# Optimization experiments

Measured on AMD Instinct MI355X. Metric: run time of the kernel, lower is better.

The kernel has to match this reference:

```python
import jax, jax.numpy as jnp
import numpy as np

EPS = 1e-5

# ---------------- numpy-side hash/index precomputation ----------------

def _key(c):
    c = c.astype(np.int64) + 2  # shift so all coords >= 0
    return (c[..., 0] * 4096 + c[..., 1]) * 4096 + c[..., 2]

def _lookup(table_keys, query_keys):
    order = np.argsort(table_keys)
    sk = table_keys[order]
    pos = np.clip(np.searchsorted(sk, query_keys), 0, len(sk) - 1)
    found = sk[pos] == query_keys
    return np.where(found, order[pos], -1).astype(np.int64)

def setup_inputs() -> dict:
    N, C_IN, C_OUT, RES = 400_000, 32, 64, 1.0
    rng = np.random.default_rng(0)
    coords = rng.uniform(0.0, 100.0, (N, 3)).astype(np.float32)
    pf = rng.standard_normal((N, C_IN)).astype(np.float32)

    # initial_voxelize: unique voxel coords + point->voxel map
    vc = np.floor(coords / RES).astype(np.int64)
    uv, p2v_in = np.unique(vc, axis=0, return_inverse=True)
    p2v_in = p2v_in.reshape(-1)
    cnt_in = np.bincount(p2v_in, minlength=len(uv)).astype(np.float32)

    # strided conv output lattice (stride 2)
    ouv = np.unique(uv // 2, axis=0)
    ikeys, okeys = _key(uv), _key(ouv)

    # kernel-2 stride-2 conv map: input voxel at 2*out + off, off in {0,1}^3
    offs2 = np.array([[i, j, k] for i in (0, 1) for j in (0, 1) for k in (0, 1)], np.int64)
    conv_map = np.stack([_lookup(ikeys, _key(ouv * 2 + o)) for o in offs2], axis=1)

    # kernel-3 neighbor map on the output lattice
    offs3 = np.array([[i, j, k] for i in (-1, 0, 1) for j in (-1, 0, 1) for k in (-1, 0, 1)], np.int64)
    nbr27 = np.stack([_lookup(okeys, _key(ouv + o)) for o in offs3], axis=1)

    # trilinear voxel_to_point on output lattice (voxel size = 2*RES)
    q = coords / (2.0 * RES)
    base = np.floor(q).astype(np.int64)
    frac = (q - base).astype(np.float32)
    tri_idx, tri_w = [], []
    for o in offs2:
        idx = _lookup(okeys, _key(base + o))
        w = np.prod(np.where(o[None, :] == 1, frac, 1.0 - frac), axis=1).astype(np.float32)
        tri_idx.append(idx)
        tri_w.append(np.where(idx >= 0, w, 0.0).astype(np.float32))
    tri_idx = np.stack(tri_idx, axis=1)
    tri_w = np.stack(tri_w, axis=1)

    # point_to_voxel: containing output voxel (always exists)
    p2v_out = _lookup(okeys, _key(base))
    cnt_out = np.bincount(p2v_out, minlength=len(ouv)).astype(np.float32)

    def glorot(r, *shape):
        fan_in = shape[-2] * int(np.prod(shape[:-2])) if len(shape) > 2 else shape[0]
        return (r.standard_normal(shape) / np.sqrt(fan_in)).astype(np.float32)

    return dict(
        pf=jnp.asarray(pf),
        Wc=jnp.asarray(glorot(rng, 8, C_IN, C_OUT)),
        g1=jnp.ones(C_OUT, jnp.float32), b1=jnp.zeros(C_OUT, jnp.float32),
        Wr1=jnp.asarray(glorot(rng, 27, C_OUT, C_OUT)),
        gr1=jnp.ones(C_OUT, jnp.float32), br1=jnp.zeros(C_OUT, jnp.float32),
        Wr2=jnp.asarray(glorot(rng, 27, C_OUT, C_OUT)),
        gr2=jnp.ones(C_OUT, jnp.float32), br2=jnp.zeros(C_OUT, jnp.float32),
        Wpt=jnp.asarray(glorot(rng, C_OUT, C_OUT)), bpt=jnp.zeros(C_OUT, jnp.float32),
        gp=jnp.ones(C_OUT, jnp.float32), bp=jnp.zeros(C_OUT, jnp.float32),
        tri_w=jnp.asarray(tri_w), cnt_in=jnp.asarray(cnt_in), cnt_out=jnp.asarray(cnt_out),
        p2v_in=jnp.asarray(p2v_in), conv_map=jnp.asarray(conv_map),
        nbr27=jnp.asarray(nbr27), tri_idx=jnp.asarray(tri_idx), p2v_out=jnp.asarray(p2v_out),
    )

# ---------------- jax forward ----------------

def _bn(x, g, b):  # training-mode batch norm over voxel/point dim
    m = x.mean(0)
    v = x.var(0)
    return (x - m) * jax.lax.rsqrt(v + EPS) * g + b

def _seg_mean(x, seg, cnt):  # spvoxelize: scatter-mean
    return jax.ops.segment_sum(x, seg, num_segments=cnt.shape[0]) / cnt[:, None]

def _sconv(f, nbr, W):  # sparse conv: per-offset gather + matmul accumulate
    out = jnp.zeros((nbr.shape[0], W.shape[2]), f.dtype)
    for k in range(W.shape[0]):
        idx = nbr[:, k]
        g = jnp.where((idx >= 0)[:, None], f[jnp.maximum(idx, 0)], 0.0)
        out = out + g @ W[k]
    return out

def _tri(f, idx, w):  # trilinear voxel->point gather (w already 0 for missing)
    out = jnp.zeros((idx.shape[0], f.shape[1]), f.dtype)
    for j in range(idx.shape[1]):
        out = out + w[:, j:j + 1] * f[jnp.maximum(idx[:, j], 0)]
    return out

def reference(pf, Wc, g1, b1, Wr1, gr1, br1, Wr2, gr2, br2, Wpt, bpt, gp, bp,
              tri_w, cnt_in, cnt_out, p2v_in, conv_map, nbr27, tri_idx, p2v_out):
    vf0 = _seg_mean(pf, p2v_in, cnt_in)                         # initial_voxelize [M_in,32]
    vf1 = jax.nn.relu(_bn(_sconv(vf0, conv_map, Wc), g1, b1))   # conv_in [M_out,64]
    pfeat = _tri(vf1, tri_idx, tri_w)                           # voxel_to_point [N,64]
    vf2 = _seg_mean(pfeat, p2v_out, cnt_out)                    # point_to_voxel [M_out,64]
    h = jax.nn.relu(_bn(_sconv(vf2, nbr27, Wr1), gr1, br1))     # ResBlock conv1
    h = jax.nn.relu(_bn(_sconv(h, nbr27, Wr2), gr2, br2))       # ResBlock conv2
    vf3 = h + vf2                                               # residual sum
    p_out = jax.nn.relu(_bn(pfeat @ Wpt + bpt, gp, bp))         # point_layer
    pfeat2 = _tri(vf3, tri_idx, tri_w) + p_out                  # v2p + fuse
    vf4 = _seg_mean(pfeat2, p2v_out, cnt_out)                   # point_to_voxel
    return vf4, pfeat2
```

## Files before the change

### kernel.cpp

```cpp
#include <hip/hip_runtime.h>

#define EPSV 1e-5f
#define CDIV(a, b) (((a) + (b) - 1) / (b))

using short8 = __attribute__((ext_vector_type(8))) short;
using f32x4 = __attribute__((ext_vector_type(4))) float;

__device__ __forceinline__ unsigned short bf16rne(float x) {
  unsigned u = __float_as_uint(x);
  unsigned r = (u + 0x7fffu + ((u >> 16) & 1u)) >> 16;
  return (unsigned short)r;
}

__global__ __launch_bounds__(256) void k_conv1(const float* __restrict__ vin,
                                               const int* __restrict__ cmap,
                                               const float* __restrict__ W,
                                               float* __restrict__ out,
                                               float* __restrict__ stats, int Vout) {
  __shared__ float fs[32][128];
  __shared__ float Ws[32 * 64];
  __shared__ int idxs[128 * 8];
  __shared__ float ss[128];
  const int tid = threadIdx.x;
  const int vb = blockIdx.x * 128;
  for (int i = tid; i < 128 * 8; i += 256) {
    int g = vb * 8 + i;
    idxs[i] = (g < Vout * 8) ? cmap[g] : -1;
  }
  if (tid < 128) ss[tid] = 0.f;
  const int vq = tid & 15, cq = tid >> 4;
  const int v0 = vq * 8, c0 = cq * 4;
  const int srow = tid & 127, sci = (tid >> 7) * 16;
  float acc[8][4];
#pragma unroll
  for (int r = 0; r < 8; ++r)
#pragma unroll
    for (int q = 0; q < 4; ++q) acc[r][q] = 0.f;

  for (int k = 0; k < 8; ++k) {
    __syncthreads();
    for (int i = tid; i < 32 * 64; i += 256) Ws[i] = W[k * 2048 + i];
    int idx = idxs[srow * 8 + k];
    if (idx >= 0) {
#pragma unroll
      for (int j = 0; j < 16; j += 4) {
        float4 t = *(const float4*)&vin[(size_t)idx * 32 + sci + j];
        fs[sci + j + 0][srow] = t.x;
        fs[sci + j + 1][srow] = t.y;
        fs[sci + j + 2][srow] = t.z;
        fs[sci + j + 3][srow] = t.w;
      }
    } else {
#pragma unroll
      for (int j = 0; j < 16; ++j) fs[sci + j][srow] = 0.f;
    }
    __syncthreads();
#pragma unroll 8
    for (int ci = 0; ci < 32; ++ci) {
      float4 w4 = *(const float4*)&Ws[ci * 64 + c0];
      float4 fa = *(const float4*)&fs[ci][v0];
      float4 fb = *(const float4*)&fs[ci][v0 + 4];
      float fv[8] = {fa.x, fa.y, fa.z, fa.w, fb.x, fb.y, fb.z, fb.w};
      float wv[4] = {w4.x, w4.y, w4.z, w4.w};
#pragma unroll
      for (int r = 0; r < 8; ++r)
#pragma unroll
        for (int q = 0; q < 4; ++q) acc[r][q] += fv[r] * wv[q];
    }
  }
  float s1[4] = {0, 0, 0, 0}, s2[4] = {0, 0, 0, 0};
#pragma unroll
  for (int r = 0; r < 8; ++r) {
    int v = vb + v0 + r;
    if (v < Vout) {
      *(float4*)&out[(size_t)v * 64 + c0] =
          make_float4(acc[r][0], acc[r][1], acc[r][2], acc[r][3]);
#pragma unroll
      for (int q = 0; q < 4; ++q) {
        float x = acc[r][q];
        s1[q] += x;
        s2[q] += x * x;
      }
    }
  }
#pragma unroll
  for (int q = 0; q < 4; ++q) {
    atomicAdd(&ss[c0 + q], s1[q]);
    atomicAdd(&ss[64 + c0 + q], s2[q]);
  }
  __syncthreads();
  if (tid < 128) atomicAdd(&stats[tid], ss[tid]);
}

__global__ void k_bnfin(const float* __restrict__ stats, const float* __restrict__ g,
                        const float* __restrict__ b, float* __restrict__ sb, int rows) {
  int c = threadIdx.x;
  float inv = 1.f / (float)rows;
  float m = stats[c] * inv;
  float v = stats[64 + c] * inv - m * m;
  float sc = g[c] * rsqrtf(v + EPSV);
  sb[c] = sc;
  sb[64 + c] = b[c] - m * sc;
}

__global__ __launch_bounds__(1024) void k_scan_part(const float* __restrict__ cnt,
                                                    int* __restrict__ partial, int V) {
  __shared__ int s[1024];
  int i = blockIdx.x * 1024 + threadIdx.x;
  s[threadIdx.x] = (i < V) ? (int)cnt[i] : 0;
  __syncthreads();
  for (int st = 512; st > 0; st >>= 1) {
    if (threadIdx.x < st) s[threadIdx.x] += s[threadIdx.x + st];
    __syncthreads();
  }
  if (threadIdx.x == 0) partial[blockIdx.x] = s[0];
}

__global__ __launch_bounds__(1024) void k_scan_top(int* __restrict__ partial, int nb) {
  __shared__ int s[1024];
  int t = threadIdx.x;
  int orig = (t < nb) ? partial[t] : 0;
  s[t] = orig;
  __syncthreads();
  for (int st = 1; st < 1024; st <<= 1) {
    int v = (t >= st) ? s[t - st] : 0;
    __syncthreads();
    s[t] += v;
    __syncthreads();
  }
  if (t < nb) partial[t] = s[t] - orig;
}

__global__ __launch_bounds__(1024) void k_scan_write(const float* __restrict__ cnt,
                                                     const int* __restrict__ partial,
                                                     int* __restrict__ starts,
                                                     int* __restrict__ cursor, int V) {
  __shared__ int s[1024];
  int t = threadIdx.x;
  int i = blockIdx.x * 1024 + t;
  int orig = (i < V) ? (int)cnt[i] : 0;
  s[t] = orig;
  __syncthreads();
  for (int st = 1; st < 1024; st <<= 1) {
    int v = (t >= st) ? s[t - st] : 0;
    __syncthreads();
    s[t] += v;
    __syncthreads();
  }
  if (i < V) {
    int excl = s[t] - orig + partial[blockIdx.x];
    starts[i] = excl;
    cursor[i] = excl;
  }
}

__global__ void k_bucket(const int* __restrict__ p2v, int* __restrict__ cursor,
                         int* __restrict__ plist, int N) {
  int p = blockIdx.x * 256 + threadIdx.x;
  if (p >= N) return;
  int pos = atomicAdd(&cursor[p2v[p]], 1);
  plist[pos] = p;
}

__global__ __launch_bounds__(256) void k_seg_gather_in(const float* __restrict__ src,
                                                       const int* __restrict__ starts,
                                                       const float* __restrict__ cnt,
                                                       const int* __restrict__ plist,
                                                       float* __restrict__ dst, int V) {
  int t = threadIdx.x;
  int v = blockIdx.x * 8 + (t >> 5);
  int c = t & 31;
  if (v >= V) return;
  int s0 = starts[v];
  int n = (int)cnt[v];
  float acc = 0.f;
  for (int i = 0; i < n; ++i) acc += src[(size_t)plist[s0 + i] * 32 + c];
  dst[(size_t)v * 32 + c] = acc / (float)n;
}

__global__ __launch_bounds__(256) void k_tri1v(const float* __restrict__ c1,
                                               const float* __restrict__ sb0,
                                               const int* __restrict__ tidx,
                                               const float* __restrict__ twt,
                                               const int* __restrict__ starts,
                                               const float* __restrict__ cnt,
                                               const int* __restrict__ plist,
                                               float* __restrict__ pfeat,
                                               float* __restrict__ vf2, int V) {
  int t = threadIdx.x;
  int v = blockIdx.x * 4 + (t >> 6);
  int c = t & 63;
  if (v >= V) return;
  int s0 = starts[v];
  int n = (int)cnt[v];
  if (n < 1) return;
  int p0 = plist[s0];
  float sc = sb0[c], bi = sb0[64 + c];
  float R[8];
#pragma unroll
  for (int j = 0; j < 8; ++j) {
    int idx = tidx[(size_t)p0 * 8 + j];
    R[j] = (idx >= 0) ? fmaxf(sc * c1[(size_t)idx * 64 + c] + bi, 0.f) : 0.f;
  }
  float acc_v = 0.f;
  for (int i = 0; i < n; ++i) {
    int p = plist[s0 + i];
    float4 w0 = *(const float4*)&twt[(size_t)p * 8];
    float4 w1 = *(const float4*)&twt[(size_t)p * 8 + 4];
    float acc = w0.x * R[0] + w0.y * R[1] + w0.z * R[2] + w0.w * R[3] +
                w1.x * R[4] + w1.y * R[5] + w1.z * R[6] + w1.w * R[7];
    pfeat[(size_t)p * 64 + c] = acc;
    acc_v += acc;
  }
  vf2[(size_t)v * 64 + c] = acc_v / (float)n;
}

__global__ void k_wprep(const float* __restrict__ W, short* __restrict__ Wh,
                        short* __restrict__ Wl, int ntap) {
  int t = blockIdx.x * 256 + threadIdx.x;
  int total = ntap * 2 * 4 * 64;
  if (t >= total) return;
  int l = t & 63;
  int n = (t >> 6) & 3;
  int s = (t >> 8) & 1;
  int k = t >> 9;
  int co = n * 16 + (l & 15);
  int ci0 = s * 32 + (l >> 4) * 8;
#pragma unroll
  for (int j = 0; j < 8; ++j) {
    float x = W[((size_t)(k * 64 + ci0 + j)) * 64 + co];
    unsigned short hb = bf16rne(x);
    float hf = __uint_as_float((unsigned)hb << 16);
    Wh[(size_t)t * 8 + j] = (short)hb;
    Wl[(size_t)t * 8 + j] = (short)bf16rne(x - hf);
  }
}

__global__ void k_split(const float* __restrict__ in, const float* __restrict__ sb,
                        short* __restrict__ packed, int total) {
  int i = blockIdx.x * 256 + threadIdx.x;
  if (i >= total) return;
  int c = i & 63;
  float x = in[i];
  if (sb) x = fmaxf(sb[c] * x + sb[64 + c], 0.f);
  unsigned short hb = bf16rne(x);
  float hf = __uint_as_float((unsigned)hb << 16);
  size_t base = (size_t)(i >> 6) * 128 + c;
  packed[base] = (short)hb;
  packed[base + 64] = (short)bf16rne(x - hf);
}

__global__ __launch_bounds__(128) void k_conv27r(const short* __restrict__ A_g,
                                                 const int* __restrict__ nbr,
                                                 const short* __restrict__ Wh,
                                                 const short* __restrict__ Wl,
                                                 float* __restrict__ out,
                                                 float* __restrict__ stats, int Vout,
                                                 int nwg) {
  __shared__ float ss[128];
  const int tid = threadIdx.x;
  const int lane = tid & 63;
  const int w = tid >> 6;
  int bid = blockIdx.x;
  int q = nwg >> 3, r = nwg & 7;
  int xcd = bid & 7, pos = bid >> 3;
  int swz = (xcd < r ? xcd * (q + 1) : r * (q + 1) + (xcd - r) * q) + pos;
  const int vb = swz * 64 + w * 32;
  ss[tid] = 0.f;
  const int vv = lane & 15, kq = lane >> 4;
  const int v0 = vb + vv, v1 = vb + 16 + vv;
  const bool ok0 = v0 < Vout, ok1 = v1 < Vout;
  const int koff = kq * 8;

  f32x4 acc[2][4];
#pragma unroll
  for (int m = 0; m < 2; ++m)
#pragma unroll
    for (int n = 0; n < 4; ++n)
#pragma unroll
      for (int rr = 0; rr < 4; ++rr) acc[m][n][rr] = 0.f;

  auto ldA = [&](int idx, int off) -> short8 {
    if (idx < 0) {
      short8 z = 0;
      return z;
    }
    return *(const short8*)&A_g[(size_t)idx * 128 + off];
  };

  short8 cA[8], nA[8];
  int idn0, idn1;

  {
    int i0 = ok0 ? nbr[(size_t)v0 * 27] : -1;
    int i1 = ok1 ? nbr[(size_t)v1 * 27] : -1;
#pragma unroll
    for (int s = 0; s < 2; ++s)
#pragma unroll
      for (int h = 0; h < 2; ++h) {
        cA[s * 2 + h] = ldA(i0, h * 64 + s * 32 + koff);
        cA[4 + s * 2 + h] = ldA(i1, h * 64 + s * 32 + koff);
      }
    idn0 = ok0 ? nbr[(size_t)v0 * 27 + 1] : -1;
    idn1 = ok1 ? nbr[(size_t)v1 * 27 + 1] : -1;
  }

  for (int k = 0; k < 27; ++k) {
    int idf0 = -1, idf1 = -1;
    if (k + 1 < 27) {
#pragma unroll
      for (int s = 0; s < 2; ++s)
#pragma unroll
        for (int h = 0; h < 2; ++h) {
          nA[s * 2 + h] = ldA(idn0, h * 64 + s * 32 + koff);
          nA[4 + s * 2 + h] = ldA(idn1, h * 64 + s * 32 + koff);
        }
      if (k + 2 < 27) {
        idf0 = ok0 ? nbr[(size_t)v0 * 27 + (k + 2)] : -1;
        idf1 = ok1 ? nbr[(size_t)v1 * 27 + (k + 2)] : -1;
      }
    }
    const short* bkh = Wh + (size_t)k * 4096 + lane * 8;
    const short* bkl = Wl + (size_t)k * 4096 + lane * 8;
#pragma unroll
    for (int s = 0; s < 2; ++s) {
      short8 ah0 = cA[s * 2], al0 = cA[s * 2 + 1];
      short8 ah1 = cA[4 + s * 2], al1 = cA[4 + s * 2 + 1];
#pragma unroll
      for (int n = 0; n < 4; ++n) {
        short8 bh = *(const short8*)&bkh[(s * 4 + n) * 512];
        short8 bl = *(const short8*)&bkl[(s * 4 + n) * 512];
        acc[0][n] = __builtin_amdgcn_mfma_f32_16x16x32_bf16(ah0, bh, acc[0][n], 0, 0, 0);
        acc[0][n] = __builtin_amdgcn_mfma_f32_16x16x32_bf16(al0, bh, acc[0][n], 0, 0, 0);
        acc[0][n] = __builtin_amdgcn_mfma_f32_16x16x32_bf16(ah0, bl, acc[0][n], 0, 0, 0);
        acc[1][n] = __builtin_amdgcn_mfma_f32_16x16x32_bf16(ah1, bh, acc[1][n], 0, 0, 0);
        acc[1][n] = __builtin_amdgcn_mfma_f32_16x16x32_bf16(al1, bh, acc[1][n], 0, 0, 0);
        acc[1][n] = __builtin_amdgcn_mfma_f32_16x16x32_bf16(ah1, bl, acc[1][n], 0, 0, 0);
      }
    }
    if (k + 1 < 27) {
#pragma unroll
      for (int qq = 0; qq < 8; ++qq) cA[qq] = nA[qq];
      idn0 = idf0;
      idn1 = idf1;
    }
  }

  const int col = lane & 15, rq = lane >> 4;
  __syncthreads();
#pragma unroll
  for (int m = 0; m < 2; ++m) {
#pragma unroll
    for (int n = 0; n < 4; ++n) {
      int c = n * 16 + col;
      float s1 = 0.f, s2 = 0.f;
#pragma unroll
      for (int rr = 0; rr < 4; ++rr) {
        int v = vb + w * 0 + m * 16 + rq * 4 + rr;
        if (v < Vout) {
          float x = acc[m][n][rr];
          out[(size_t)v * 64 + c] = x;
          s1 += x;
          s2 += x * x;
        }
      }
      atomicAdd(&ss[c], s1);
      atomicAdd(&ss[64 + c], s2);
    }
  }
  __syncthreads();
  atomicAdd(&stats[tid], ss[tid]);
}

__global__ void k_vf3(const float* __restrict__ h2, const float* __restrict__ vf2,
                      const float* __restrict__ sb2, float* __restrict__ vf3, int total) {
  int i = blockIdx.x * 256 + threadIdx.x;
  if (i >= total) return;
  int c = i & 63;
  vf3[i] = fmaxf(sb2[c] * h2[i] + sb2[64 + c], 0.f) + vf2[i];
}

__global__ __launch_bounds__(256) void k_pmm(const float* __restrict__ pfeat,
                                             const float* __restrict__ Wpt,
                                             const float* __restrict__ bpt,
                                             float* __restrict__ outbuf,
                                             float* __restrict__ stats, int N) {
  __shared__ float fs[64][128];
  __shared__ float Ws[64 * 64];
  __shared__ float ss[128];
  const int tid = threadIdx.x;
  const int pb = blockIdx.x * 128;
  for (int i = tid; i < 64 * 64; i += 256) Ws[i] = Wpt[i];
  if (tid < 128) ss[tid] = 0.f;
  const int srow = tid & 127, sci = (tid >> 7) * 32;
  int p = pb + srow;
  if (p < N) {
#pragma unroll
    for (int j = 0; j < 32; j += 4) {
      float4 t = *(const float4*)&pfeat[(size_t)p * 64 + sci + j];
      fs[sci + j + 0][srow] = t.x;
      fs[sci + j + 1][srow] = t.y;
      fs[sci + j + 2][srow] = t.z;
      fs[sci + j + 3][srow] = t.w;
    }
  } else {
#pragma unroll
    for (int j = 0; j < 32; ++j) fs[sci + j][srow] = 0.f;
  }
  __syncthreads();
  const int vq = tid & 15, cq = tid >> 4;
  const int p0 = vq * 8, c0 = cq * 4;
  float acc[8][4];
#pragma unroll
  for (int r = 0; r < 8; ++r)
#pragma unroll
    for (int q = 0; q < 4; ++q) acc[r][q] = 0.f;
#pragma unroll 8
  for (int ci = 0; ci < 64; ++ci) {
    float4 w4 = *(const float4*)&Ws[ci * 64 + c0];
    float4 fa = *(const float4*)&fs[ci][p0];
    float4 fb = *(const float4*)&fs[ci][p0 + 4];
    float fv[8] = {fa.x, fa.y, fa.z, fa.w, fb.x, fb.y, fb.z, fb.w};
    float wv[4] = {w4.x, w4.y, w4.z, w4.w};
#pragma unroll
    for (int r = 0; r < 8; ++r)
#pragma unroll
      for (int q = 0; q < 4; ++q) acc[r][q] += fv[r] * wv[q];
  }
  float bb[4] = {bpt[c0], bpt[c0 + 1], bpt[c0 + 2], bpt[c0 + 3]};
  float s1[4] = {0, 0, 0, 0}, s2[4] = {0, 0, 0, 0};
#pragma unroll
  for (int r = 0; r < 8; ++r) {
    int pp = pb + p0 + r;
    if (pp < N) {
      float4 o;
      o.x = acc[r][0] + bb[0];
      o.y = acc[r][1] + bb[1];
      o.z = acc[r][2] + bb[2];
      o.w = acc[r][3] + bb[3];
      *(float4*)&outbuf[(size_t)pp * 64 + c0] = o;
      s1[0] += o.x; s2[0] += o.x * o.x;
      s1[1] += o.y; s2[1] += o.y * o.y;
      s1[2] += o.z; s2[2] += o.z * o.z;
      s1[3] += o.w; s2[3] += o.w * o.w;
    }
  }
#pragma unroll
  for (int q = 0; q < 4; ++q) {
    atomicAdd(&ss[c0 + q], s1[q]);
    atomicAdd(&ss[64 + c0 + q], s2[q]);
  }
  __syncthreads();
  if (tid < 128) atomicAdd(&stats[tid], ss[tid]);
}

__global__ __launch_bounds__(256) void k_tri2v(const float* __restrict__ vf3,
                                               const float* __restrict__ sb3,
                                               const int* __restrict__ tidx,
                                               const float* __restrict__ twt,
                                               const int* __restrict__ starts,
                                               const float* __restrict__ cnt,
                                               const int* __restrict__ plist,
                                               float* __restrict__ pf2,
                                               float* __restrict__ vf4, int V) {
  int t = threadIdx.x;
  int v = blockIdx.x * 4 + (t >> 6);
  int c = t & 63;
  if (v >= V) return;
  int s0 = starts[v];
  int n = (int)cnt[v];
  if (n < 1) return;
  int p0 = plist[s0];
  float S[8];
#pragma unroll
  for (int j = 0; j < 8; ++j) {
    int idx = tidx[(size_t)p0 * 8 + j];
    S[j] = (idx >= 0) ? vf3[(size_t)idx * 64 + c] : 0.f;
  }
  float s3 = sb3[c], b3 = sb3[64 + c];
  float acc_v = 0.f;
  for (int i = 0; i < n; ++i) {
    int p = plist[s0 + i];
    float4 w0 = *(const float4*)&twt[(size_t)p * 8];
    float4 w1 = *(const float4*)&twt[(size_t)p * 8 + 4];
    float raw = pf2[(size_t)p * 64 + c];
    float val = fmaxf(s3 * raw + b3, 0.f) +
                w0.x * S[0] + w0.y * S[1] + w0.z * S[2] + w0.w * S[3] +
                w1.x * S[4] + w1.y * S[5] + w1.z * S[6] + w1.w * S[7];
    pf2[(size_t)p * 64 + c] = val;
    acc_v += val;
  }
  vf4[(size_t)v * 64 + c] = acc_v / (float)n;
}

extern "C" void kernel_launch(void* const* d_in, const int* in_sizes, int n_in,
                              void* d_out, int out_size, void* d_ws, size_t ws_size,
                              hipStream_t stream) {
  const float* pf = (const float*)d_in[0];
  const float* Wc = (const float*)d_in[1];
  const float* g1 = (const float*)d_in[2];
  const float* b1 = (const float*)d_in[3];
  const float* Wr1 = (const float*)d_in[4];
  const float* gr1 = (const float*)d_in[5];
  const float* br1 = (const float*)d_in[6];
  const float* Wr2 = (const float*)d_in[7];
  const float* gr2 = (const float*)d_in[8];
  const float* br2 = (const float*)d_in[9];
  const float* Wpt = (const float*)d_in[10];
  const float* bpt = (const float*)d_in[11];
  const float* gp = (const float*)d_in[12];
  const float* bp = (const float*)d_in[13];
  const float* twt = (const float*)d_in[14];
  const float* cnt_in = (const float*)d_in[15];
  const float* cnt_out = (const float*)d_in[16];
  const int* p2v_in = (const int*)d_in[17];
  const int* conv_map = (const int*)d_in[18];
  const int* nbr27 = (const int*)d_in[19];
  const int* tri_idx = (const int*)d_in[20];
  const int* p2v_out = (const int*)d_in[21];

  const int N = in_sizes[0] / 32;
  const int Vin = in_sizes[15];
  const int Vout = in_sizes[16];

  float* ws = (float*)d_ws;
  size_t o = 0;
  auto alloc = [&](size_t nf) {
    float* pbase = ws + o;
    o += (nf + 63) & ~(size_t)63;
    return pbase;
  };
  size_t vf0_sz = (size_t)Vin * 32;
  size_t vf3_sz = (size_t)Vout * 64;
  float* vf0 = alloc(vf0_sz > vf3_sz ? vf0_sz : vf3_sz);
  float* c1 = alloc((size_t)Vout * 64);
  float* pfeat = alloc((size_t)N * 64);
  float* vf2 = alloc((size_t)Vout * 64);
  float* h1 = alloc((size_t)Vout * 64);
  float* stats = alloc(512);
  float* sb = alloc(512);
  int* partial = (int*)alloc(1024);
  int* starts = (int*)alloc(Vout);
  int* cursor = (int*)alloc(Vout);
  int* plist = (int*)alloc(N);
  int* starts_in = (int*)alloc(Vin);
  int* cursor_in = (int*)alloc(Vin);
  int* plist_in = (int*)alloc(N);
  const int WFRAG = 27 * 2 * 4 * 64 * 8;
  short* Wh1 = (short*)alloc(WFRAG / 2);
  short* Wl1 = (short*)alloc(WFRAG / 2);
  short* Wh2 = (short*)alloc(WFRAG / 2);
  short* Wl2 = (short*)alloc(WFRAG / 2);
  float* vf3 = vf0;
  float* h2 = c1;
  short* vf2p = (short*)pfeat;
  short* h1p = vf2p + (size_t)Vout * 128;

  float* vf4 = (float*)d_out;
  float* pf2 = vf4 + (size_t)Vout * 64;

  const int nb_out = CDIV(Vout, 1024);
  const int nb_in = CDIV(Vin, 1024);
  const int nwg27 = CDIV(Vout, 64);

  hipMemsetAsync(stats, 0, 512 * sizeof(float), stream);

  k_scan_part<<<nb_in, 1024, 0, stream>>>(cnt_in, partial, Vin);
  k_scan_top<<<1, 1024, 0, stream>>>(partial, nb_in);
  k_scan_write<<<nb_in, 1024, 0, stream>>>(cnt_in, partial, starts_in, cursor_in, Vin);
  k_bucket<<<CDIV(N, 256), 256, 0, stream>>>(p2v_in, cursor_in, plist_in, N);
  k_seg_gather_in<<<CDIV(Vin, 8), 256, 0, stream>>>(pf, starts_in, cnt_in, plist_in,
                                                    vf0, Vin);

  k_conv1<<<CDIV(Vout, 128), 256, 0, stream>>>(vf0, conv_map, Wc, c1, stats, Vout);
  k_bnfin<<<1, 64, 0, stream>>>(stats, g1, b1, sb, Vout);

  k_scan_part<<<nb_out, 1024, 0, stream>>>(cnt_out, partial, Vout);
  k_scan_top<<<1, 1024, 0, stream>>>(partial, nb_out);
  k_scan_write<<<nb_out, 1024, 0, stream>>>(cnt_out, partial, starts, cursor, Vout);
  k_bucket<<<CDIV(N, 256), 256, 0, stream>>>(p2v_out, cursor, plist, N);

  k_wprep<<<CDIV(27 * 2 * 4 * 64, 256), 256, 0, stream>>>(Wr1, Wh1, Wl1, 27);
  k_wprep<<<CDIV(27 * 2 * 4 * 64, 256), 256, 0, stream>>>(Wr2, Wh2, Wl2, 27);

  k_tri1v<<<CDIV(Vout, 4), 256, 0, stream>>>(c1, sb, tri_idx, twt, starts, cnt_out,
                                             plist, pfeat, vf2, Vout);

  k_pmm<<<CDIV(N, 128), 256, 0, stream>>>(pfeat, Wpt, bpt, pf2, stats + 384, N);
  k_bnfin<<<1, 64, 0, stream>>>(stats + 384, gp, bp, sb + 384, N);

  k_split<<<CDIV(Vout * 64, 256), 256, 0, stream>>>(vf2, nullptr, vf2p, Vout * 64);
  k_conv27r<<<nwg27, 128, 0, stream>>>(vf2p, nbr27, Wh1, Wl1, h1, stats + 128, Vout,
                                       nwg27);
  k_bnfin<<<1, 64, 0, stream>>>(stats + 128, gr1, br1, sb + 128, Vout);

  k_split<<<CDIV(Vout * 64, 256), 256, 0, stream>>>(h1, sb + 128, h1p, Vout * 64);
  k_conv27r<<<nwg27, 128, 0, stream>>>(h1p, nbr27, Wh2, Wl2, h2, stats + 256, Vout,
                                       nwg27);
  k_bnfin<<<1, 64, 0, stream>>>(stats + 256, gr2, br2, sb + 256, Vout);

  k_vf3<<<CDIV(Vout * 64, 256), 256, 0, stream>>>(h2, vf2, sb + 256, vf3, Vout * 64);

  k_tri2v<<<CDIV(Vout, 4), 256, 0, stream>>>(vf3, sb + 384, tri_idx, twt, starts,
                                             cnt_out, plist, pf2, vf4, Vout);
}
```

Before: 1.311 ms.

## Widen conv27 tile to 64 voxels per wave with double-buffered tap loads

Each wave of the 27-tap residual conv now computes 64 output voxels (4 M-tiles) instead of 32, so each weight fragment loaded from global memory feeds twice as many MFMAs. The tap loop is manually unrolled by two with ping-pong A buffers, prefetching the next tap's gathered features while the current tap's MFMAs run. Launch bounds request 2 blocks per CU and the grid halves. The trade-off is much higher VGPR use (32 short8 A registers plus 16 accumulators), which lowers occupancy and could cause spills.

New measurement: 1.244 ms. 1.05x faster.

```diff
diff --git a/kernel.cpp b/kernel.cpp
--- a/kernel.cpp
+++ b/kernel.cpp
@@ -250,13 +250,48 @@
   packed[base + 64] = (short)bf16rne(x - hf);
 }
 
-__global__ __launch_bounds__(128) void k_conv27r(const short* __restrict__ A_g,
-                                                 const int* __restrict__ nbr,
-                                                 const short* __restrict__ Wh,
-                                                 const short* __restrict__ Wl,
-                                                 float* __restrict__ out,
-                                                 float* __restrict__ stats, int Vout,
-                                                 int nwg) {
+#define TAP_LOAD(NXT, kk)                                                        \
+  {                                                                              \
+    _Pragma("unroll") for (int m = 0; m < 4; ++m) {                              \
+      _Pragma("unroll") for (int s = 0; s < 2; ++s) {                            \
+        _Pragma("unroll") for (int h = 0; h < 2; ++h) {                          \
+          NXT[m * 4 + s * 2 + h] = ldA(idxn[m], h * 64 + s * 32 + koff);         \
+        }                                                                        \
+      }                                                                          \
+    }                                                                            \
+    _Pragma("unroll") for (int m = 0; m < 4; ++m) {                              \
+      idxn[m] = (ok[m] && (kk) + 2 < 27) ? nbr[(size_t)vm[m] * 27 + (kk) + 2]    \
+                                         : -1;                                   \
+    }                                                                            \
+  }
+
+#define TAP_MFMA(CUR, kk)                                                        \
+  {                                                                              \
+    const short* bkh = Wh + (size_t)(kk)*4096 + lane * 8;                        \
+    const short* bkl = Wl + (size_t)(kk)*4096 + lane * 8;                        \
+    _Pragma("unroll") for (int s = 0; s < 2; ++s) {                              \
+      _Pragma("unroll") for (int n = 0; n < 4; ++n) {                            \
+        short8 bh = *(const short8*)&bkh[(s * 4 + n) * 512];                     \
+        short8 bl = *(const short8*)&bkl[(s * 4 + n) * 512];                     \
+        _Pragma("unroll") for (int m = 0; m < 4; ++m) {                          \
+          acc[m][n] = __builtin_amdgcn_mfma_f32_16x16x32_bf16(                   \
+              CUR[m * 4 + s * 2], bh, acc[m][n], 0, 0, 0);                       \
+          acc[m][n] = __builtin_amdgcn_mfma_f32_16x16x32_bf16(                   \
+              CUR[m * 4 + s * 2 + 1], bh, acc[m][n], 0, 0, 0);                   \
+          acc[m][n] = __builtin_amdgcn_mfma_f32_16x16x32_bf16(                   \
+              CUR[m * 4 + s * 2], bl, acc[m][n], 0, 0, 0);                       \
+        }                                                                        \
+      }                                                                          \
+    }                                                                            \
+  }
+
+__global__ __launch_bounds__(128, 2) void k_conv27r(const short* __restrict__ A_g,
+                                                    const int* __restrict__ nbr,
+                                                    const short* __restrict__ Wh,
+                                                    const short* __restrict__ Wl,
+                                                    float* __restrict__ out,
+                                                    float* __restrict__ stats, int Vout,
+                                                    int nwg) {
   __shared__ float ss[128];
   const int tid = threadIdx.x;
   const int lane = tid & 63;
@@ -265,16 +300,21 @@
   int q = nwg >> 3, r = nwg & 7;
   int xcd = bid & 7, pos = bid >> 3;
   int swz = (xcd < r ? xcd * (q + 1) : r * (q + 1) + (xcd - r) * q) + pos;
-  const int vb = swz * 64 + w * 32;
+  const int vb = swz * 128 + w * 64;
   ss[tid] = 0.f;
   const int vv = lane & 15, kq = lane >> 4;
-  const int v0 = vb + vv, v1 = vb + 16 + vv;
-  const bool ok0 = v0 < Vout, ok1 = v1 < Vout;
   const int koff = kq * 8;
-
-  f32x4 acc[2][4];
-#pragma unroll
-  for (int m = 0; m < 2; ++m)
+  int vm[4];
+  bool ok[4];
+#pragma unroll
+  for (int m = 0; m < 4; ++m) {
+    vm[m] = vb + m * 16 + vv;
+    ok[m] = vm[m] < Vout;
+  }
+
+  f32x4 acc[4][4];
+#pragma unroll
+  for (int m = 0; m < 4; ++m)
 #pragma unroll
     for (int n = 0; n < 4; ++n)
 #pragma unroll
@@ -288,75 +328,40 @@
     return *(const short8*)&A_g[(size_t)idx * 128 + off];
   };
 
-  short8 cA[8], nA[8];
-  int idn0, idn1;
-
-  {
-    int i0 = ok0 ? nbr[(size_t)v0 * 27] : -1;
-    int i1 = ok1 ? nbr[(size_t)v1 * 27] : -1;
+  short8 A0[16], A1[16];
+  int idxn[4];
+
+#pragma unroll
+  for (int m = 0; m < 4; ++m) idxn[m] = ok[m] ? nbr[(size_t)vm[m] * 27] : -1;
+#pragma unroll
+  for (int m = 0; m < 4; ++m)
 #pragma unroll
     for (int s = 0; s < 2; ++s)
 #pragma unroll
-      for (int h = 0; h < 2; ++h) {
-        cA[s * 2 + h] = ldA(i0, h * 64 + s * 32 + koff);
-        cA[4 + s * 2 + h] = ldA(i1, h * 64 + s * 32 + koff);
-      }
-    idn0 = ok0 ? nbr[(size_t)v0 * 27 + 1] : -1;
-    idn1 = ok1 ? nbr[(size_t)v1 * 27 + 1] : -1;
-  }
-
-  for (int k = 0; k < 27; ++k) {
-    int idf0 = -1, idf1 = -1;
-    if (k + 1 < 27) {
-#pragma unroll
-      for (int s = 0; s < 2; ++s)
-#pragma unroll
-        for (int h = 0; h < 2; ++h) {
-          nA[s * 2 + h] = ldA(idn0, h * 64 + s * 32 + koff);
-          nA[4 + s * 2 + h] = ldA(idn1, h * 64 + s * 32 + koff);
-        }
-      if (k + 2 < 27) {
-        idf0 = ok0 ? nbr[(size_t)v0 * 27 + (k + 2)] : -1;
-        idf1 = ok1 ? nbr[(size_t)v1 * 27 + (k + 2)] : -1;
-      }
-    }
-    const short* bkh = Wh + (size_t)k * 4096 + lane * 8;
-    const short* bkl = Wl + (size_t)k * 4096 + lane * 8;
-#pragma unroll
-    for (int s = 0; s < 2; ++s) {
-      short8 ah0 = cA[s * 2], al0 = cA[s * 2 + 1];
-      short8 ah1 = cA[4 + s * 2], al1 = cA[4 + s * 2 + 1];
-#pragma unroll
-      for (int n = 0; n < 4; ++n) {
-        short8 bh = *(const short8*)&bkh[(s * 4 + n) * 512];
-        short8 bl = *(const short8*)&bkl[(s * 4 + n) * 512];
-        acc[0][n] = __builtin_amdgcn_mfma_f32_16x16x32_bf16(ah0, bh, acc[0][n], 0, 0, 0);
-        acc[0][n] = __builtin_amdgcn_mfma_f32_16x16x32_bf16(al0, bh, acc[0][n], 0, 0, 0);
-        acc[0][n] = __builtin_amdgcn_mfma_f32_16x16x32_bf16(ah0, bl, acc[0][n], 0, 0, 0);
-        acc[1][n] = __builtin_amdgcn_mfma_f32_16x16x32_bf16(ah1, bh, acc[1][n], 0, 0, 0);
-        acc[1][n] = __builtin_amdgcn_mfma_f32_16x16x32_bf16(al1, bh, acc[1][n], 0, 0, 0);
-        acc[1][n] = __builtin_amdgcn_mfma_f32_16x16x32_bf16(ah1, bl, acc[1][n], 0, 0, 0);
-      }
-    }
-    if (k + 1 < 27) {
-#pragma unroll
-      for (int qq = 0; qq < 8; ++qq) cA[qq] = nA[qq];
-      idn0 = idf0;
-      idn1 = idf1;
-    }
-  }
+      for (int h = 0; h < 2; ++h)
+        A0[m * 4 + s * 2 + h] = ldA(idxn[m], h * 64 + s * 32 + koff);
+#pragma unroll
+  for (int m = 0; m < 4; ++m) idxn[m] = ok[m] ? nbr[(size_t)vm[m] * 27 + 1] : -1;
+
+  for (int kk = 0; kk < 26; kk += 2) {
+    TAP_LOAD(A1, kk);
+    TAP_MFMA(A0, kk);
+    TAP_LOAD(A0, kk + 1);
+    TAP_MFMA(A1, kk + 1);
+  }
+  TAP_MFMA(A0, 26);
 
   const int col = lane & 15, rq = lane >> 4;
   __syncthreads();
 #pragma unroll
-  for (int m = 0; m < 2; ++m) {
+  for (int m = 0; m < 4; ++m) {
 #pragma unroll
     for (int n = 0; n < 4; ++n) {
       int c = n * 16 + col;
       float s1 = 0.f, s2 = 0.f;
 #pragma unroll
       for (int rr = 0; rr < 4; ++rr) {
-        int v = vb + w * 0 + m * 16 + rq * 4 + rr;
+        int v = vb + m * 16 + rq * 4 + rr;
         if (v < Vout) {
           float x = acc[m][n][rr];
           out[(size_t)v * 64 + c] = x;
@@ -561,7 +566,7 @@
 
   const int nb_out = CDIV(Vout, 1024);
   const int nb_in = CDIV(Vin, 1024);
-  const int nwg27 = CDIV(Vout, 64);
+  const int nwg27 = CDIV(Vout, 128);
 
   hipMemsetAsync(stats, 0, 512 * sizeof(float), stream);
 
```
